# Optimization experiments

Measured on AMD Instinct MI355X. Metric: run time of the kernel, lower is better.

## Reference

```python
import jax, jax.numpy as jnp
import numpy as np

B, N, DIM = 8, 1024, 1024
HEADS, DIM_HEAD = 16, 64
INNER = HEADS * DIM_HEAD  # 1024


def setup_inputs() -> dict:
    key = jax.random.key(0)
    k1, k2, k3 = jax.random.split(key, 3)
    x = jax.random.normal(k1, (B, N, DIM), dtype=jnp.float32)
    # Dense kernels (Glorot-ish scale for numerical sanity)
    w_qkv = jax.random.normal(k2, (DIM, 3 * INNER), dtype=jnp.float32) * (DIM ** -0.5)
    w_out = jax.random.normal(k3, (INNER, DIM), dtype=jnp.float32) * (INNER ** -0.5)
    b_out = jnp.zeros((DIM,), dtype=jnp.float32)
    return {"x": x, "w_qkv": w_qkv, "w_out": w_out, "b_out": b_out}


def reference(x, w_qkv, w_out, b_out):
    scale = DIM_HEAD ** -0.5
    qkv = x @ w_qkv                                   # [B, N, 3*INNER]
    q, k, v = jnp.split(qkv, 3, axis=-1)              # each [B, N, INNER]

    def to_heads(t):
        # [B, N, H*Dh] -> [B, H, N, Dh]
        return t.reshape(B, N, HEADS, DIM_HEAD).transpose(0, 2, 1, 3)

    q, k, v = to_heads(q), to_heads(k), to_heads(v)
    dots = jnp.einsum("bhid,bhjd->bhij", q, k) * scale   # [B, H, N, N]
    attn = jax.nn.softmax(dots, axis=-1)
    out = jnp.einsum("bhij,bhjd->bhid", attn, v)          # [B, H, N, Dh]
    out = out.transpose(0, 2, 1, 3).reshape(B, N, INNER)  # merge heads
    return out @ w_out + b_out                            # project_out (dropout inactive at inference)
```

## Files before the change

### kernel.cpp

```cpp
#include <hip/hip_runtime.h>
#include <hip/hip_bf16.h>
#include <math.h>

typedef __bf16 bf16_t;
typedef __bf16 bf16x8 __attribute__((ext_vector_type(8)));
typedef float f32x4 __attribute__((ext_vector_type(4)));

#define LOG2E 1.44269504088896340736f

#define GL2LDS(g, l)                                                     \
  __builtin_amdgcn_global_load_lds(                                      \
      (const __attribute__((address_space(1))) unsigned int*)(g),        \
      (__attribute__((address_space(3))) unsigned int*)(l), 16, 0, 0)

#define BAR() asm volatile("s_barrier" ::: "memory")
#define VMCNT(n) asm volatile("s_waitcnt vmcnt(" #n ")" ::: "memory")
#define LGKM0()                                         \
  do {                                                  \
    asm volatile("s_waitcnt lgkmcnt(0)" ::: "memory");  \
    __builtin_amdgcn_sched_barrier(0);                  \
  } while (0)

__global__ __launch_bounds__(256) void convert_f32_bf16(const float* __restrict__ in,
                                                        bf16_t* __restrict__ out) {
  const size_t idx = (size_t)(blockIdx.x * 256 + threadIdx.x) * 8;
  f32x4 a = *(const f32x4*)&in[idx];
  f32x4 b = *(const f32x4*)&in[idx + 4];
  bf16x8 v;
#pragma unroll
  for (int i = 0; i < 4; i++) { v[i] = (bf16_t)a[i]; v[i + 4] = (bf16_t)b[i]; }
  *(bf16x8*)&out[idx] = v;
}

__global__ __launch_bounds__(256) void transpose_f32_bf16(const float* __restrict__ in,
                                                          bf16_t* __restrict__ out,
                                                          int R, int C) {
  __shared__ bf16_t t[64][65];
  const int c0 = blockIdx.x * 64, r0 = blockIdx.y * 64;
  const int tx = threadIdx.x, ty = threadIdx.y;
#pragma unroll
  for (int i = 0; i < 16; i++) {
    int r = ty + i * 4;
    t[r][tx] = (bf16_t)in[(size_t)(r0 + r) * C + c0 + tx];
  }
  __syncthreads();
#pragma unroll
  for (int i = 0; i < 16; i++) {
    int r = ty + i * 4;
    out[(size_t)(c0 + r) * R + r0 + tx] = t[tx][r];
  }
}

template <int MODE>
__global__ __launch_bounds__(256, 4) void gemmT(const bf16_t* __restrict__ A,
                                                const bf16_t* __restrict__ Bt,
                                                bf16_t* __restrict__ Qb,
                                                bf16_t* __restrict__ Kb,
                                                bf16_t* __restrict__ Vtb,
                                                const float* __restrict__ bias,
                                                float* __restrict__ Out) {
  constexpr int K = 1024;
  constexpr int NT = K / 32;
  __shared__ __align__(16) bf16_t As[3][128 * 32];
  __shared__ __align__(16) bf16_t Bs[3][128 * 32];
  const int gx = gridDim.x;
  const int lin = blockIdx.y * gx + blockIdx.x;
  const int per = (gx * gridDim.y) >> 3;
  const int swz = (lin & 7) * per + (lin >> 3);
  const int m0 = (swz / gx) * 128, n0 = (swz % gx) * 128;
  const int tid = threadIdx.x;
  const int w = tid >> 6, l = tid & 63;
  const int lr = l & 15, lq = l >> 4;
  const int wm = w >> 1, wn = w & 1;

  const int rs = tid >> 2, ps = tid & 3;
  const int cs = (ps ^ ((rs >> 1) & 3)) * 8;
  const size_t gA0 = (size_t)(m0 + rs) * K + cs;
  const size_t gA1 = (size_t)(m0 + 64 + rs) * K + cs;
  const size_t gB0 = (size_t)(n0 + rs) * K + cs;
  const size_t gB1 = (size_t)(n0 + 64 + rs) * K + cs;
  const int ldsu0 = (w * 64) * 8;
  const int ldsu1 = (256 + w * 64) * 8;

#define STG(bf_, kt_)                                   \
  do {                                                  \
    const size_t kk_ = (size_t)(kt_) * 32;              \
    GL2LDS(&A[gA0 + kk_], &As[bf_][ldsu0]);             \
    GL2LDS(&A[gA1 + kk_], &As[bf_][ldsu1]);             \
    GL2LDS(&Bt[gB0 + kk_], &Bs[bf_][ldsu0]);            \
    GL2LDS(&Bt[gB1 + kk_], &Bs[bf_][ldsu1]);            \
  } while (0)

  int aoff[4], boff[4];
#pragma unroll
  for (int mf = 0; mf < 4; mf++) {
    const int row = wm * 64 + mf * 16 + lr;
    aoff[mf] = row * 32 + ((lq ^ ((row >> 1) & 3)) << 3);
  }
#pragma unroll
  for (int nf = 0; nf < 4; nf++) {
    const int row = wn * 64 + nf * 16 + lr;
    boff[nf] = row * 32 + ((lq ^ ((row >> 1) & 3)) << 3);
  }

  f32x4 acc[4][4] = {};

  STG(0, 0);
  STG(1, 1);
  VMCNT(4);
  BAR();

  for (int t = 0; t < NT; ++t) {
    const int bufR = t % 3;
    if (t + 2 < NT) STG((t + 2) % 3, t + 2);
    bf16x8 af[4], bv[4];
#pragma unroll
    for (int mf = 0; mf < 4; mf++)
      af[mf] = *(const bf16x8*)&As[bufR][aoff[mf]];
#pragma unroll
    for (int nf = 0; nf < 4; nf++)
      bv[nf] = *(const bf16x8*)&Bs[bufR][boff[nf]];
    LGKM0();
    __builtin_amdgcn_s_setprio(1);
#pragma unroll
    for (int mf = 0; mf < 4; mf++)
#pragma unroll
      for (int nf = 0; nf < 4; nf++)
        acc[mf][nf] = __builtin_amdgcn_mfma_f32_16x16x32_bf16(af[mf], bv[nf],
                                                              acc[mf][nf], 0, 0, 0);
    __builtin_amdgcn_s_setprio(0);
    if (t == NT - 2) { VMCNT(0); } else if (t < NT - 2) { VMCNT(4); }
    BAR();
  }

#pragma unroll
  for (int mf = 0; mf < 4; mf++)
#pragma unroll
    for (int nf = 0; nf < 4; nf++)
#pragma unroll
      for (int i = 0; i < 4; i++) {
        const int m = m0 + wm * 64 + mf * 16 + lq * 4 + i;
        const int c = n0 + wn * 64 + nf * 16 + lr;
        const float v = acc[mf][nf][i];
        if (MODE == 1) {
          Out[(size_t)m * 1024 + c] = v + bias[c];
        } else {
          const int b = m >> 10, n = m & 1023;
          const int which = c >> 10, cc = c & 1023;
          const int hh = cc >> 6, d = cc & 63;
          const size_t qk = ((size_t)((b * 16 + hh) * 1024 + n)) * 64 + d;
          if (which == 0)
            Qb[qk] = (bf16_t)(v * (0.125f * LOG2E));
          else if (which == 1)
            Kb[qk] = (bf16_t)v;
          else
            Vtb[((size_t)((b * 16 + hh) * 64 + d)) * 1024 + n] = (bf16_t)v;
        }
      }
}

#define KVS 68
#define PS  72
__global__ __launch_bounds__(256) void attn128(const bf16_t* __restrict__ Qb,
                                               const bf16_t* __restrict__ Kb,
                                               const bf16_t* __restrict__ Vtb,
                                               bf16_t* __restrict__ Ob) {
  __shared__ __align__(16) bf16_t Ks[2][64 * KVS];
  __shared__ __align__(16) bf16_t Vs[2][64 * KVS];
  __shared__ __align__(16) bf16_t Pl[4 * 32 * PS];
  const int bid = blockIdx.x;
  const int qt = bid & 7, h = (bid >> 3) & 15, b = bid >> 7;
  const bf16_t* Qh = Qb + (size_t)((b * 16 + h) * 1024) * 64;
  const bf16_t* Kh = Kb + (size_t)((b * 16 + h) * 1024) * 64;
  const bf16_t* Vh = Vtb + (size_t)((b * 16 + h) * 64) * 1024;
  const int tid = threadIdx.x, w = tid >> 6, l = tid & 63;
  const int lr = l & 15, lq = l >> 4;
  const int q0 = qt * 128 + w * 32;

  bf16x8 onesf;
#pragma unroll
  for (int i = 0; i < 8; i++) onesf[i] = (lr == 0) ? (bf16_t)1.0f : (bf16_t)0.0f;

  const int sr = tid >> 3, sc = tid & 7;

  bf16x8 qf[2][2];
#pragma unroll
  for (int mt = 0; mt < 2; mt++)
#pragma unroll
    for (int ks = 0; ks < 2; ks++)
      qf[mt][ks] = *(const bf16x8*)&Qh[(size_t)(q0 + mt * 16 + lr) * 64 + ks * 32 + lq * 8];

  {
    bf16x8 k0 = *(const bf16x8*)&Kh[(size_t)sr * 64 + sc * 8];
    bf16x8 k1 = *(const bf16x8*)&Kh[(size_t)(sr + 32) * 64 + sc * 8];
    bf16x8 v0 = *(const bf16x8*)&Vh[(size_t)sr * 1024 + sc * 8];
    bf16x8 v1 = *(const bf16x8*)&Vh[(size_t)(sr + 32) * 1024 + sc * 8];
    *(bf16x8*)&Ks[0][sr * KVS + sc * 8] = k0;
    *(bf16x8*)&Ks[0][(sr + 32) * KVS + sc * 8] = k1;
    *(bf16x8*)&Vs[0][sr * KVS + sc * 8] = v0;
    *(bf16x8*)&Vs[0][(sr + 32) * KVS + sc * 8] = v1;
  }
  __syncthreads();

  f32x4 o[2][4] = {};
  f32x4 o5[2] = {};
  bf16_t* pw = &Pl[w * 32 * PS];

  for (int it = 0; it < 16; ++it) {
    const int buf = it & 1;
    bf16x8 nk0, nk1, nv0, nv1;
    if (it < 15) {
      const int jn = (it + 1) * 64;
      nk0 = *(const bf16x8*)&Kh[(size_t)(jn + sr) * 64 + sc * 8];
      nk1 = *(const bf16x8*)&Kh[(size_t)(jn + sr + 32) * 64 + sc * 8];
      nv0 = *(const bf16x8*)&Vh[(size_t)sr * 1024 + jn + sc * 8];
      nv1 = *(const bf16x8*)&Vh[(size_t)(sr + 32) * 1024 + jn + sc * 8];
    }
    f32x4 s[2][4] = {};
#pragma unroll
    for (int ks = 0; ks < 2; ks++)
#pragma unroll
      for (int nt = 0; nt < 4; nt++) {
        bf16x8 kf = *(const bf16x8*)&Ks[buf][(nt * 16 + lr) * KVS + ks * 32 + lq * 8];
#pragma unroll
        for (int mt = 0; mt < 2; mt++)
          s[mt][nt] = __builtin_amdgcn_mfma_f32_16x16x32_bf16(qf[mt][ks], kf, s[mt][nt], 0, 0, 0);
      }
#pragma unroll
    for (int mt = 0; mt < 2; mt++)
#pragma unroll
      for (int nt = 0; nt < 4; nt++)
#pragma unroll
        for (int i = 0; i < 4; i++)
          pw[(mt * 16 + lq * 4 + i) * PS + nt * 16 + lr] = (bf16_t)exp2f(s[mt][nt][i]);
#pragma unroll
    for (int ks = 0; ks < 2; ks++) {
      bf16x8 af[2];
#pragma unroll
      for (int mt = 0; mt < 2; mt++)
        af[mt] = *(const bf16x8*)&pw[(mt * 16 + lr) * PS + ks * 32 + lq * 8];
#pragma unroll
      for (int nt = 0; nt < 4; nt++) {
        bf16x8 vf = *(const bf16x8*)&Vs[buf][(nt * 16 + lr) * KVS + ks * 32 + lq * 8];
#pragma unroll
        for (int mt = 0; mt < 2; mt++)
          o[mt][nt] = __builtin_amdgcn_mfma_f32_16x16x32_bf16(af[mt], vf, o[mt][nt], 0, 0, 0);
      }
#pragma unroll
      for (int mt = 0; mt < 2; mt++)
        o5[mt] = __builtin_amdgcn_mfma_f32_16x16x32_bf16(af[mt], onesf, o5[mt], 0, 0, 0);
    }
    if (it < 15) {
      *(bf16x8*)&Ks[buf ^ 1][sr * KVS + sc * 8] = nk0;
      *(bf16x8*)&Ks[buf ^ 1][(sr + 32) * KVS + sc * 8] = nk1;
      *(bf16x8*)&Vs[buf ^ 1][sr * KVS + sc * 8] = nv0;
      *(bf16x8*)&Vs[buf ^ 1][(sr + 32) * KVS + sc * 8] = nv1;
    }
    __syncthreads();
  }
#pragma unroll
  for (int mt = 0; mt < 2; mt++)
#pragma unroll
    for (int i = 0; i < 4; i++) {
      float lsum = __shfl(o5[mt][i], lq * 16);
      float inv = 1.0f / lsum;
      int grow = b * 1024 + q0 + mt * 16 + lq * 4 + i;
#pragma unroll
      for (int nt = 0; nt < 4; nt++) {
        int col = h * 64 + nt * 16 + lr;
        Ob[(size_t)grow * 1024 + col] = (bf16_t)(o[mt][nt][i] * inv);
      }
    }
}

extern "C" void kernel_launch(void* const* d_in, const int* in_sizes, int n_in,
                              void* d_out, int out_size, void* d_ws, size_t ws_size,
                              hipStream_t stream) {
  const float* x     = (const float*)d_in[0];
  const float* w_qkv = (const float*)d_in[1];
  const float* w_out = (const float*)d_in[2];
  const float* b_out = (const float*)d_in[3];
  float* out = (float*)d_out;

  bf16_t* ws = (bf16_t*)d_ws;
  const size_t SZ = (size_t)8 * 1024 * 1024;
  bf16_t* Qb  = ws;
  bf16_t* Kb  = Qb + SZ;
  bf16_t* Vtb = Kb + SZ;
  bf16_t* Ob  = Vtb + SZ;
  bf16_t* Wqt = Ob + SZ;
  bf16_t* Wot = Wqt + (size_t)3072 * 1024;
  bf16_t* Xb  = Ob;

  hipLaunchKernelGGL(convert_f32_bf16, dim3(4096), dim3(256), 0, stream, x, Xb);
  hipLaunchKernelGGL(transpose_f32_bf16, dim3(48, 16), dim3(64, 4), 0, stream,
                     w_qkv, Wqt, 1024, 3072);
  hipLaunchKernelGGL(transpose_f32_bf16, dim3(16, 16), dim3(64, 4), 0, stream,
                     w_out, Wot, 1024, 1024);
  hipLaunchKernelGGL((gemmT<0>), dim3(24, 64), dim3(256), 0, stream,
                     Xb, Wqt, Qb, Kb, Vtb, (const float*)nullptr, (float*)nullptr);
  hipLaunchKernelGGL(attn128, dim3(1024), dim3(256), 0, stream, Qb, Kb, Vtb, Ob);
  hipLaunchKernelGGL((gemmT<1>), dim3(8, 64), dim3(256), 0, stream,
                     Ob, Wot, (bf16_t*)nullptr, (bf16_t*)nullptr, (bf16_t*)nullptr,
                     b_out, out);
}
```

Measured before the change: 279.9 us.

## Transpose attention MFMAs so P and O are stored as packed row vectors

The QK^T and PV MFMAs now take K/V as the A operand and Q/P as the B operand. Each lane therefore holds four consecutive key columns of one query row, so P is written to LDS as bf16x4 with an XOR swizzle instead of scalar stores. The output is also written as bf16x4, the row sum is read from the accumulator without a shuffle, and the block index order is changed so consecutive blocks cover different heads. The intent is to cut LDS store instructions, bank conflicts and scattered global stores, at the cost of more complex indexing.

```diff
diff --git a/kernel.cpp b/kernel.cpp
--- a/kernel.cpp
+++ b/kernel.cpp
@@ -3,6 +3,7 @@
 #include <math.h>
 
 typedef __bf16 bf16_t;
+typedef __bf16 bf16x4 __attribute__((ext_vector_type(4)));
 typedef __bf16 bf16x8 __attribute__((ext_vector_type(8)));
 typedef float f32x4 __attribute__((ext_vector_type(4)));
 
@@ -169,26 +170,27 @@
   __shared__ __align__(16) bf16_t Vs[2][64 * KVS];
   __shared__ __align__(16) bf16_t Pl[4 * 32 * PS];
   const int bid = blockIdx.x;
-  const int qt = bid & 7, h = (bid >> 3) & 15, b = bid >> 7;
+  const int qt = bid >> 7, b = (bid >> 4) & 7, h = bid & 15;
   const bf16_t* Qh = Qb + (size_t)((b * 16 + h) * 1024) * 64;
   const bf16_t* Kh = Kb + (size_t)((b * 16 + h) * 1024) * 64;
   const bf16_t* Vh = Vtb + (size_t)((b * 16 + h) * 64) * 1024;
   const int tid = threadIdx.x, w = tid >> 6, l = tid & 63;
   const int lr = l & 15, lq = l >> 4;
   const int q0 = qt * 128 + w * 32;
-
-  bf16x8 onesf;
-#pragma unroll
-  for (int i = 0; i < 8; i++) onesf[i] = (lr == 0) ? (bf16_t)1.0f : (bf16_t)0.0f;
+  const int swz = (lr >> 1) & 3;
+
+  bf16x8 onesA;
+#pragma unroll
+  for (int i = 0; i < 8; i++) onesA[i] = (bf16_t)1.0f;
 
   const int sr = tid >> 3, sc = tid & 7;
 
   bf16x8 qf[2][2];
 #pragma unroll
-  for (int mt = 0; mt < 2; mt++)
+  for (int mf = 0; mf < 2; mf++)
 #pragma unroll
     for (int ks = 0; ks < 2; ks++)
-      qf[mt][ks] = *(const bf16x8*)&Qh[(size_t)(q0 + mt * 16 + lr) * 64 + ks * 32 + lq * 8];
+      qf[mf][ks] = *(const bf16x8*)&Qh[(size_t)(q0 + mf * 16 + lr) * 64 + ks * 32 + lq * 8];
 
   {
     bf16x8 k0 = *(const bf16x8*)&Kh[(size_t)sr * 64 + sc * 8];
@@ -202,7 +204,7 @@
   }
   __syncthreads();
 
-  f32x4 o[2][4] = {};
+  f32x4 o[4][2] = {};
   f32x4 o5[2] = {};
   bf16_t* pw = &Pl[w * 32 * PS];
 
@@ -216,39 +218,42 @@
       nv0 = *(const bf16x8*)&Vh[(size_t)sr * 1024 + jn + sc * 8];
       nv1 = *(const bf16x8*)&Vh[(size_t)(sr + 32) * 1024 + jn + sc * 8];
     }
-    f32x4 s[2][4] = {};
+    f32x4 s[4][2] = {};
 #pragma unroll
     for (int ks = 0; ks < 2; ks++)
 #pragma unroll
-      for (int nt = 0; nt < 4; nt++) {
-        bf16x8 kf = *(const bf16x8*)&Ks[buf][(nt * 16 + lr) * KVS + ks * 32 + lq * 8];
-#pragma unroll
-        for (int mt = 0; mt < 2; mt++)
-          s[mt][nt] = __builtin_amdgcn_mfma_f32_16x16x32_bf16(qf[mt][ks], kf, s[mt][nt], 0, 0, 0);
+      for (int nf = 0; nf < 4; nf++) {
+        bf16x8 kf = *(const bf16x8*)&Ks[buf][(nf * 16 + lr) * KVS + ks * 32 + lq * 8];
+#pragma unroll
+        for (int mf = 0; mf < 2; mf++)
+          s[nf][mf] = __builtin_amdgcn_mfma_f32_16x16x32_bf16(kf, qf[mf][ks], s[nf][mf], 0, 0, 0);
       }
 #pragma unroll
-    for (int mt = 0; mt < 2; mt++)
-#pragma unroll
-      for (int nt = 0; nt < 4; nt++)
-#pragma unroll
-        for (int i = 0; i < 4; i++)
-          pw[(mt * 16 + lq * 4 + i) * PS + nt * 16 + lr] = (bf16_t)exp2f(s[mt][nt][i]);
+    for (int mf = 0; mf < 2; mf++)
+#pragma unroll
+      for (int nf = 0; nf < 4; nf++) {
+        bf16x4 pk;
+#pragma unroll
+        for (int i = 0; i < 4; i++) pk[i] = (bf16_t)exp2f(s[nf][mf][i]);
+        *(bf16x4*)&pw[(mf * 16 + lr) * PS + (((nf * 2 + (lq >> 1)) ^ swz) << 3) +
+                      (lq & 1) * 4] = pk;
+      }
 #pragma unroll
     for (int ks = 0; ks < 2; ks++) {
-      bf16x8 af[2];
-#pragma unroll
-      for (int mt = 0; mt < 2; mt++)
-        af[mt] = *(const bf16x8*)&pw[(mt * 16 + lr) * PS + ks * 32 + lq * 8];
-#pragma unroll
-      for (int nt = 0; nt < 4; nt++) {
-        bf16x8 vf = *(const bf16x8*)&Vs[buf][(nt * 16 + lr) * KVS + ks * 32 + lq * 8];
-#pragma unroll
-        for (int mt = 0; mt < 2; mt++)
-          o[mt][nt] = __builtin_amdgcn_mfma_f32_16x16x32_bf16(af[mt], vf, o[mt][nt], 0, 0, 0);
+      bf16x8 pf[2];
+#pragma unroll
+      for (int mf = 0; mf < 2; mf++)
+        pf[mf] = *(const bf16x8*)&pw[(mf * 16 + lr) * PS + ((ks * 4 + (lq ^ swz)) << 3)];
+#pragma unroll
+      for (int df = 0; df < 4; df++) {
+        bf16x8 vf = *(const bf16x8*)&Vs[buf][(df * 16 + lr) * KVS + ks * 32 + lq * 8];
+#pragma unroll
+        for (int mf = 0; mf < 2; mf++)
+          o[df][mf] = __builtin_amdgcn_mfma_f32_16x16x32_bf16(vf, pf[mf], o[df][mf], 0, 0, 0);
       }
 #pragma unroll
-      for (int mt = 0; mt < 2; mt++)
-        o5[mt] = __builtin_amdgcn_mfma_f32_16x16x32_bf16(af[mt], onesf, o5[mt], 0, 0, 0);
+      for (int mf = 0; mf < 2; mf++)
+        o5[mf] = __builtin_amdgcn_mfma_f32_16x16x32_bf16(onesA, pf[mf], o5[mf], 0, 0, 0);
     }
     if (it < 15) {
       *(bf16x8*)&Ks[buf ^ 1][sr * KVS + sc * 8] = nk0;
@@ -259,18 +264,17 @@
     __syncthreads();
   }
 #pragma unroll
-  for (int mt = 0; mt < 2; mt++)
-#pragma unroll
-    for (int i = 0; i < 4; i++) {
-      float lsum = __shfl(o5[mt][i], lq * 16);
-      float inv = 1.0f / lsum;
-      int grow = b * 1024 + q0 + mt * 16 + lq * 4 + i;
-#pragma unroll
-      for (int nt = 0; nt < 4; nt++) {
-        int col = h * 64 + nt * 16 + lr;
-        Ob[(size_t)grow * 1024 + col] = (bf16_t)(o[mt][nt][i] * inv);
-      }
+  for (int mf = 0; mf < 2; mf++) {
+    const float inv = 1.0f / o5[mf][0];
+    const int grow = b * 1024 + q0 + mf * 16 + lr;
+#pragma unroll
+    for (int df = 0; df < 4; df++) {
+      bf16x4 ov;
+#pragma unroll
+      for (int i = 0; i < 4; i++) ov[i] = (bf16_t)(o[df][mf][i] * inv);
+      *(bf16x4*)&Ob[(size_t)grow * 1024 + h * 64 + df * 16 + lq * 4] = ov;
     }
+  }
 }
 
 extern "C" void kernel_launch(void* const* d_in, const int* in_sizes, int n_in,
```

Result: no change. 283.6 us (+1.3%).
